# Kernel optimization log

Measured on AMD Instinct MI355X. Metric: run time of the kernel, lower is better.

The kernel has to match this reference:

```python
import jax, jax.numpy as jnp
import numpy as np

N_BUILDINGS = 4096
NUM_CLUSTERS = 128
EMBED_DIM = 128
TEMPORAL_DIM = 24


def setup_inputs() -> dict:
    key = jax.random.key(0)
    ks = jax.random.split(key, 12)
    E, N, C, T = EMBED_DIM, N_BUILDINGS, NUM_CLUSTERS, TEMPORAL_DIM

    def lin(k, fi, fo):
        k1, k2 = jax.random.split(k)
        w = jax.random.normal(k1, (fo, fi), jnp.float32) / np.sqrt(fi).astype(np.float32)
        b = jax.random.normal(k2, (fo,), jnp.float32) * 0.01
        return w, b

    fp_w1, fp_b1 = lin(ks[0], 2 * E + 2, 128)
    fp_w2, fp_b2 = lin(ks[1], 128, 64)
    fp_w3, fp_b3 = lin(ks[2], 64, 1)
    en_w1, en_b1 = lin(ks[3], 1, 16)
    en_w2, en_b2 = lin(ks[4], 16, 1)
    ps_w1, ps_b1 = lin(ks[5], E, 32)
    ps_w2, ps_b2 = lin(ks[6], 32, 1)

    embeddings = jax.random.normal(ks[7], (1, N, E), jnp.float32)
    generation = jax.random.uniform(ks[8], (1, N, T), jnp.float32) * 50.0
    consumption = jax.random.uniform(ks[9], (1, N, T), jnp.float32) * 50.0
    positions = jax.random.uniform(ks[10], (1, N, 2), jnp.float32) * 1000.0
    cluster_assignments = (jnp.arange(N) % C)[None, :].astype(jnp.int32)

    return dict(embeddings=embeddings, generation=generation, consumption=consumption,
                positions=positions,
                fp_w1=fp_w1, fp_b1=fp_b1, fp_w2=fp_w2, fp_b2=fp_b2, fp_w3=fp_w3, fp_b3=fp_b3,
                en_w1=en_w1, en_b1=en_b1, en_w2=en_w2, en_b2=en_b2,
                ps_w1=ps_w1, ps_b1=ps_b1, ps_w2=ps_w2, ps_b2=ps_b2,
                cluster_assignments=cluster_assignments, num_clusters=C, current_hour=12)


def _greedy_cluster(net0, prio, effm, pf):
    """Greedy allocation within one cluster. net0,prio: [K]; effm,pf: [K,K].
    Surplus rows and deficit cols are both visited in descending priority order;
    non-surplus rows have avail=0 and non-deficit cols have needed<=0, matching the
    original code's subset selection + break/continue semantics."""
    K = net0.shape[0]
    order = jnp.argsort(-prio)
    inv = jnp.argsort(order)
    net_o = net0[order]
    eff_o = effm[order][:, order]
    pf_o = pf[order][:, order]

    def outer(dnet, i):
        avail0 = jnp.maximum(net_o[i], 0.0)  # surplus net is never mutated

        def inner(carry, j):
            avail, dn = carry
            needed = -dn[j]
            active = (avail > 0.0) & (needed > 0.0)
            f = jnp.where(active, jnp.minimum(jnp.minimum(avail, needed), pf_o[i, j]), 0.0)
            dn = dn.at[j].add(f * eff_o[i, j])  # deficit receives delivered flow
            return (avail - f, dn), (f, active)

        (_, dnet), (frow, arow) = jax.lax.scan(inner, (avail0, dnet), jnp.arange(K))
        return dnet, (frow, arow)

    dnet, (flows_o, act_o) = jax.lax.scan(outer, net_o, jnp.arange(K))
    return flows_o[inv][:, inv], act_o[inv][:, inv], dnet[inv]


def _forward(embeddings, generation, consumption, positions,
             fp_w1, fp_b1, fp_w2, fp_b2, fp_w3, fp_b3,
             en_w1, en_b1, en_w2, en_b2,
             ps_w1, ps_b1, ps_w2, ps_b2,
             cluster_assignments, num_clusters, current_hour):
    B, N, E = embeddings.shape
    C = num_clusters
    K = N // C
    net = generation[0, :, current_hour] - consumption[0, :, current_hour]  # [N]

    g = jnp.argsort(cluster_assignments[0]).reshape(C, K)  # [C,K] building ids per cluster
    emb_c = embeddings[0][g]   # [C,K,E]
    pos_c = positions[0][g]    # [C,K,2]
    net_c = net[g]             # [C,K]

    # priority scorer (eval mode)
    h = jax.nn.relu(emb_c @ ps_w1.T + ps_b1)
    prio_c = jax.nn.sigmoid(h @ ps_w2.T + ps_b2)[..., 0]  # [C,K]

    # pairwise distances within cluster
    dist = jnp.linalg.norm(pos_c[:, :, None, :] - pos_c[:, None, :, :], axis=-1)  # [C,K,K]

    # efficiency net: eff = 0.85 + 0.13*sigmoid(MLP(dist/1000))
    eh = jax.nn.relu((dist / 1000.0)[..., None] * en_w1[:, 0] + en_b1)  # [C,K,K,16]
    eff = 0.85 + 0.13 * jax.nn.sigmoid(eh @ en_w2.T + en_b2)[..., 0]    # [C,K,K]

    # flow predictor on concat([emb_i, emb_j, dist, hour/24]); split W1 to avoid
    # materializing the [C,K,K,2E+2] feature tensor. Dropout is eval-mode identity.
    W1a, W1b = fp_w1[:, :E], fp_w1[:, E:2 * E]
    w1d, w1h = fp_w1[:, 2 * E], fp_w1[:, 2 * E + 1]
    hi = emb_c @ W1a.T  # [C,K,128]
    hj = emb_c @ W1b.T  # [C,K,128]
    hour_f = current_hour / 24.0
    h1 = jax.nn.relu(hi[:, :, None, :] + hj[:, None, :, :] + dist[..., None] * w1d + hour_f * w1h + fp_b1)
    h2 = jax.nn.relu(h1 @ fp_w2.T + fp_b2)
    pflow = jax.nn.softplus(h2 @ fp_w3.T + fp_b3)[..., 0]  # [C,K,K]

    flows_c, act_c, dnet_c = jax.vmap(_greedy_cluster)(net_c, prio_c, eff, pflow)

    sharing = jnp.zeros((N, N), embeddings.dtype).at[g[:, :, None], g[:, None, :]].set(flows_c)
    effmat = jnp.ones((N, N), embeddings.dtype).at[g[:, :, None], g[:, None, :]].set(
        jnp.where(act_c, eff, 1.0))
    net_after = jnp.zeros((N,), embeddings.dtype).at[g].set(dnet_c)

    sharing = sharing[None]
    effmat = effmat[None]
    total_shared = sharing.sum()
    energy_sent = sharing.sum(axis=2)
    energy_received = (sharing * effmat).sum(axis=1)
    return sharing, effmat, total_shared, energy_sent, energy_received, net_after[None]


def reference(embeddings, generation, consumption, positions,
              fp_w1, fp_b1, fp_w2, fp_b2, fp_w3, fp_b3,
              en_w1, en_b1, en_w2, en_b2,
              ps_w1, ps_b1, ps_w2, ps_b2,
              cluster_assignments, num_clusters, current_hour):
    return _forward(embeddings, generation, consumption, positions,
                    fp_w1, fp_b1, fp_w2, fp_b2, fp_w3, fp_b3,
                    en_w1, en_b1, en_w2, en_b2,
                    ps_w1, ps_b1, ps_w2, ps_b2,
                    cluster_assignments, num_clusters, current_hour)
```

## Files before the change

### kernel.cpp

```cpp
#include <hip/hip_runtime.h>
#include <math.h>

#define NB 4096
#define NC 128
#define NK 32
#define NE 128

typedef __bf16 bf16x8 __attribute__((ext_vector_type(8)));
typedef float floatx4 __attribute__((ext_vector_type(4)));

__device__ __forceinline__ float sigmoidf_(float x){
  if (x >= 0.f){ float z = expf(-x); return 1.f/(1.f+z); }
  float z = expf(x); return z/(1.f+z);
}
__device__ __forceinline__ float softplusf_(float x){
  return fmaxf(x, 0.f) + log1pf(expf(-fabsf(x)));
}
__device__ __forceinline__ unsigned int pack_bf16(float a, float b){
  unsigned short ua = __builtin_bit_cast(unsigned short, (__bf16)a);
  unsigned short ub = __builtin_bit_cast(unsigned short, (__bf16)b);
  return (unsigned int)ua | ((unsigned int)ub << 16);
}

__global__ void k_prep_group(const float* __restrict__ fp_w1, const float* __restrict__ ps_w1,
                             const float* __restrict__ fp_b1, const float* __restrict__ fp_w2,
                             const int* __restrict__ assign, const int* __restrict__ hourp,
                             float* __restrict__ w1at, float* __restrict__ w1bt,
                             float* __restrict__ ps_w1t, int* __restrict__ g,
                             int* __restrict__ row_of, float* __restrict__ w1d_c,
                             float* __restrict__ bzc, uint4* __restrict__ w2f,
                             float* __restrict__ total){
  int bid = blockIdx.x;
  int t = threadIdx.x;
  if (bid < 80){
    int idx = bid*256 + t;
    if (idx < 128*128){
      int o = idx >> 7, e = idx & 127;
      w1at[e*128 + o] = fp_w1[o*258 + e];
      w1bt[e*128 + o] = fp_w1[o*258 + 128 + e];
    } else {
      int i2 = idx - 128*128;
      if (i2 < 128*32){
        int e = i2 >> 5, q = i2 & 31;
        ps_w1t[e*32 + q] = ps_w1[q*128 + e];
      }
    }
  } else if (bid < 96){
    __shared__ int hist[NC];
    __shared__ int loc[256];
    int start = (bid - 80)*256;
    for (int c = t; c < NC; c += 256) hist[c] = 0;
    __syncthreads();
    for (int j = t; j < start; j += 256) atomicAdd(&hist[assign[j]], 1);
    int i = start + t;
    int c = assign[i];
    loc[t] = c;
    __syncthreads();
    int r = hist[c];
    for (int j = 0; j < 256; ++j) r += (j < t && loc[j] == c) ? 1 : 0;
    if (r >= NK) r = NK - 1;
    g[c*NK + r] = i;
    row_of[i] = c*NK + r;
  } else if (bid == 96){
    if (t < 128){
      float hour_f = (float)hourp[0] / 24.0f;
      w1d_c[t] = fp_w1[t*258 + 256];
      bzc[t]   = fmaf(hour_f, fp_w1[t*258 + 257], fp_b1[t]);
    }
    if (t == 128) total[0] = 0.f;
  } else {
    for (int ff = t; ff < 1024; ff += 256){
      int lane = ff & 63, fi = ff >> 6;
      int nt = fi >> 2, ks = fi & 3;
      int o = nt*16 + (lane & 15);
      int kb = ks*32 + (lane >> 4)*8;
      const float* src = fp_w2 + o*128 + kb;
      uint4 u;
      u.x = pack_bf16(src[0], src[1]);
      u.y = pack_bf16(src[2], src[3]);
      u.z = pack_bf16(src[4], src[5]);
      u.w = pack_bf16(src[6], src[7]);
      w2f[ff] = u;
    }
  }
}

__global__ void k_prio(const float* __restrict__ emb, const float* __restrict__ gen,
                       const float* __restrict__ cons, const float* __restrict__ pos,
                       const float* __restrict__ ps_w1t, const float* __restrict__ ps_b1,
                       const float* __restrict__ ps_w2, const float* __restrict__ ps_b2,
                       const int* __restrict__ row_of, const int* __restrict__ hourp,
                       float* __restrict__ net_c, float* __restrict__ prio_c,
                       float* __restrict__ pos_c){
  __shared__ float es[8*128];
  __shared__ float ws[128*32];
  int t = threadIdx.x;
  int i0 = blockIdx.x*8;
  for (int idx = t; idx < 8*128; idx += 256) es[idx] = emb[i0*128 + idx];
  for (int idx = t; idx < 128*32; idx += 256) ws[idx] = ps_w1t[idx];
  __syncthreads();
  int bl = t >> 5, q = t & 31;
  int i = i0 + bl;
  float acc = ps_b1[q];
  const float* er = &es[bl*128];
  for (int e = 0; e < 128; ++e) acc = fmaf(er[e], ws[e*32 + q], acc);
  float v = fmaxf(acc, 0.f) * ps_w2[q];
  for (int m = 16; m >= 1; m >>= 1) v += __shfl_xor(v, m, 32);
  if (q == 0){
    int ck = row_of[i];
    prio_c[ck] = sigmoidf_(v + ps_b2[0]);
    int h = hourp[0];
    net_c[ck] = gen[i*24 + h] - cons[i*24 + h];
    pos_c[2*ck]   = pos[2*i];
    pos_c[2*ck+1] = pos[2*i+1];
  }
}

__global__ void k_hij(const float* __restrict__ emb, const float* __restrict__ w1at,
                      const float* __restrict__ w1bt, const int* __restrict__ row_of,
                      float* __restrict__ hi_c, float* __restrict__ hj_c){
  __shared__ float es[16*132];
  int t = threadIdx.x;
  int i0 = blockIdx.x*16;
  for (int idx = t; idx < 16*128; idx += 256){
    int b = idx >> 7, e = idx & 127;
    es[b*132 + e] = emb[(i0 + b)*128 + e];
  }
  __syncthreads();
  int o = t & 127, half = t >> 7;
  float ai[8], aj[8];
#pragma unroll
  for (int r = 0; r < 8; ++r){ ai[r] = 0.f; aj[r] = 0.f; }
  for (int e = 0; e < 128; e += 4){
    float wa0 = w1at[(e+0)*128 + o], wa1 = w1at[(e+1)*128 + o];
    float wa2 = w1at[(e+2)*128 + o], wa3 = w1at[(e+3)*128 + o];
    float wb0 = w1bt[(e+0)*128 + o], wb1 = w1bt[(e+1)*128 + o];
    float wb2 = w1bt[(e+2)*128 + o], wb3 = w1bt[(e+3)*128 + o];
#pragma unroll
    for (int r = 0; r < 8; ++r){
      float4 ev = *(const float4*)&es[(half*8 + r)*132 + e];
      ai[r] = fmaf(ev.x, wa0, fmaf(ev.y, wa1, fmaf(ev.z, wa2, fmaf(ev.w, wa3, ai[r]))));
      aj[r] = fmaf(ev.x, wb0, fmaf(ev.y, wb1, fmaf(ev.z, wb2, fmaf(ev.w, wb3, aj[r]))));
    }
  }
#pragma unroll
  for (int r = 0; r < 8; ++r){
    int b = i0 + half*8 + r;
    int ck = row_of[b];
    hi_c[ck*128 + o] = ai[r];
    hj_c[ck*128 + o] = aj[r];
  }
}

__global__ __launch_bounds__(256) void k_pflow(
    const float* __restrict__ hi_c, const float* __restrict__ hj_c,
    const float* __restrict__ pos_c, const float* __restrict__ w1d_c,
    const float* __restrict__ bzc, const uint4* __restrict__ w2f,
    const float* __restrict__ fp_b2, const float* __restrict__ fp_w3,
    const float* __restrict__ fp_b3, float* __restrict__ pflow){
  int t = threadIdx.x;
  int lane = t & 63, wv = t >> 6;
  int gw = blockIdx.x*4 + wv;
  int c = gw >> 6;
  int rem = gw & 63;
  int i = rem >> 1, j0 = (rem & 1)*16;
  int l16 = lane & 15, quad = lane >> 4;
  int j = j0 + l16;
  float xi = pos_c[(c*NK + i)*2 + 0], yi = pos_c[(c*NK + i)*2 + 1];
  float xj = pos_c[(c*NK + j)*2 + 0], yj = pos_c[(c*NK + j)*2 + 1];
  float dx = xi - xj, dy = yi - yj;
  float d = sqrtf(fmaf(dx, dx, dy*dy));
  const float4* hi4 = (const float4*)(hi_c + (c*NK + i)*128);
  const float4* hj4 = (const float4*)(hj_c + (c*NK + j)*128);
  const float4* wd4 = (const float4*)w1d_c;
  const float4* bz4 = (const float4*)bzc;
  bf16x8 af[4];
#pragma unroll
  for (int ks = 0; ks < 4; ++ks){
    int q8 = ks*8 + quad*2;
    float4 a0 = hi4[q8], a1 = hi4[q8 + 1];
    float4 b0 = hj4[q8], b1 = hj4[q8 + 1];
    float4 w0 = wd4[q8], w1 = wd4[q8 + 1];
    float4 z0 = bz4[q8], z1 = bz4[q8 + 1];
    float v0 = fmaxf(a0.x + b0.x + fmaf(d, w0.x, z0.x), 0.f);
    float v1 = fmaxf(a0.y + b0.y + fmaf(d, w0.y, z0.y), 0.f);
    float v2 = fmaxf(a0.z + b0.z + fmaf(d, w0.z, z0.z), 0.f);
    float v3 = fmaxf(a0.w + b0.w + fmaf(d, w0.w, z0.w), 0.f);
    float v4 = fmaxf(a1.x + b1.x + fmaf(d, w1.x, z1.x), 0.f);
    float v5 = fmaxf(a1.y + b1.y + fmaf(d, w1.y, z1.y), 0.f);
    float v6 = fmaxf(a1.z + b1.z + fmaf(d, w1.z, z1.z), 0.f);
    float v7 = fmaxf(a1.w + b1.w + fmaf(d, w1.w, z1.w), 0.f);
    uint4 u;
    u.x = pack_bf16(v0, v1);
    u.y = pack_bf16(v2, v3);
    u.z = pack_bf16(v4, v5);
    u.w = pack_bf16(v6, v7);
    af[ks] = __builtin_bit_cast(bf16x8, u);
  }
  bf16x8 bfr[4][4];
#pragma unroll
  for (int nt = 0; nt < 4; ++nt)
#pragma unroll
    for (int ks = 0; ks < 4; ++ks)
      bfr[nt][ks] = __builtin_bit_cast(bf16x8, w2f[(nt*4 + ks)*64 + lane]);
  floatx4 acc[4];
#pragma unroll
  for (int nt = 0; nt < 4; ++nt){
    acc[nt] = (floatx4){0.f, 0.f, 0.f, 0.f};
#pragma unroll
    for (int ks = 0; ks < 4; ++ks)
      acc[nt] = __builtin_amdgcn_mfma_f32_16x16x32_bf16(af[ks], bfr[nt][ks], acc[nt], 0, 0, 0);
  }
  float b2v[4], w3v[4];
#pragma unroll
  for (int nt = 0; nt < 4; ++nt){
    b2v[nt] = fp_b2[nt*16 + l16];
    w3v[nt] = fp_w3[nt*16 + l16];
  }
  float b3 = fp_b3[0];
#pragma unroll
  for (int r = 0; r < 4; ++r){
    float s = 0.f;
#pragma unroll
    for (int nt = 0; nt < 4; ++nt)
      s = fmaf(fmaxf(acc[nt][r] + b2v[nt], 0.f), w3v[nt], s);
#pragma unroll
    for (int m = 8; m >= 1; m >>= 1) s += __shfl_xor(s, m);
    if (l16 == 0)
      pflow[c*1024 + i*32 + j0 + quad*4 + r] = softplusf_(s + b3);
  }
}

__global__ __launch_bounds__(64) void k_greedy(
    const float* __restrict__ net_c, const float* __restrict__ prio_c,
    const float* __restrict__ pos_c, const float* __restrict__ en_w1,
    const float* __restrict__ en_b1, const float* __restrict__ en_w2,
    const float* __restrict__ en_b2, const float* __restrict__ pflow,
    const int* __restrict__ g,
    float* __restrict__ fl_c, float* __restrict__ ef_c, float* __restrict__ total,
    float* __restrict__ esent, float* __restrict__ erecv, float* __restrict__ nafter){
  __shared__ float pf_s[1024];
  __shared__ float ef_s[1024];
  __shared__ float fl_s[1024];
  __shared__ float efm_s[1024];
  __shared__ float px[32], py[32];
  __shared__ int order_s[32];
  __shared__ int gl[32];
  int t = threadIdx.x;
  int tl = t & 31;
  int c = blockIdx.x;
  for (int e = t; e < 1024; e += 64) pf_s[e] = pflow[c*1024 + e];
  if (t < 32){
    float2 p2 = ((const float2*)pos_c)[c*NK + t];
    px[t] = p2.x; py[t] = p2.y;
    gl[t] = g[c*NK + t];
  }
  __syncthreads();
  for (int e = t; e < 1024; e += 64){
    int ii = e >> 5, jj = e & 31;
    float dx = px[ii] - px[jj], dy = py[ii] - py[jj];
    float d = sqrtf(fmaf(dx, dx, dy*dy));
    float ds = d * (1.0f/1000.0f);
    float acc = en_b2[0];
#pragma unroll
    for (int q = 0; q < 16; ++q)
      acc = fmaf(fmaxf(fmaf(ds, en_w1[q], en_b1[q]), 0.f), en_w2[q], acc);
    ef_s[e] = 0.85f + 0.13f*sigmoidf_(acc);
  }
  float p = (t < 32) ? prio_c[c*NK + t] : -1e30f;
  int rank = 0;
  for (int k = 0; k < 32; ++k){
    float pk = __shfl(p, k, 32);
    rank += ((pk > p) || (pk == p && k < tl)) ? 1 : 0;
  }
  if (t < 32) order_s[rank] = t;
  __syncthreads();
  int b = order_s[tl];
  float net0 = net_c[c*NK + b];
  float dnet = net0;
  float recv = 0.f;
  float ctotal = 0.f;
  for (int i = 0; i < 32; ++i){
    int a = order_s[i];
    float av0 = fmaxf(__shfl(net0, i, 32), 0.f);
    float pf = pf_s[a*32 + b];
    float ef = ef_s[a*32 + b];
    float needed = -dnet;
    float m = (needed > 0.f) ? fminf(needed, pf) : 0.f;
    float s = m;
#pragma unroll
    for (int dd = 1; dd < 32; dd <<= 1){
      float u = __shfl_up(s, dd, 32);
      if (tl >= dd) s += u;
    }
    float Se = __shfl_up(s, 1, 32);
    if (tl == 0) Se = 0.f;
    float rprev = fmaxf(av0 - Se, 0.f);
    int act = (rprev > 0.f) && (needed > 0.f);
    float f = fminf(m, rprev);
    dnet = fmaf(f, ef, dnet);
    recv = fmaf(f, ef, recv);
    if (t < 32){
      fl_s[a*32 + b]  = f;
      efm_s[a*32 + b] = act ? ef : 1.0f;
    }
    float rs = f;
    for (int mm = 16; mm >= 1; mm >>= 1) rs += __shfl_xor(rs, mm, 32);
    if (t == 0){ esent[gl[a]] = rs; ctotal += rs; }
  }
  if (t < 32){
    nafter[gl[b]] = dnet;
    erecv[gl[b]]  = recv;
  }
  if (t == 0) atomicAdd(total, ctotal);
  __syncthreads();
  for (int e = t; e < 1024; e += 64){
    fl_c[c*1024 + e] = fl_s[e];
    ef_c[c*1024 + e] = efm_s[e];
  }
}

__global__ __launch_bounds__(256) void k_write(
    const float* __restrict__ fl_c, const float* __restrict__ ef_c,
    const int* __restrict__ g, const int* __restrict__ row_of,
    float* __restrict__ sharing, float* __restrict__ effm){
  __shared__ float rowS[4096];
  __shared__ float rowE[4096];
  __shared__ int   cols[32];
  __shared__ float vals[32];
  __shared__ float vale[32];
  int t = threadIdx.x;
  int r = blockIdx.x;
  int ra = row_of[r];
  int c = ra >> 5, a = ra & 31;
  if (t < 32){
    cols[t] = g[c*NK + t];
    vals[t] = fl_c[c*1024 + a*32 + t];
    vale[t] = ef_c[c*1024 + a*32 + t];
  }
  float4 z4 = make_float4(0.f, 0.f, 0.f, 0.f);
  float4 o4 = make_float4(1.f, 1.f, 1.f, 1.f);
  float4* s4 = (float4*)rowS;
  float4* e4 = (float4*)rowE;
#pragma unroll
  for (int q = 0; q < 4; ++q){ s4[t + 256*q] = z4; e4[t + 256*q] = o4; }
  __syncthreads();
  if (t < 32){ rowS[cols[t]] = vals[t]; rowE[cols[t]] = vale[t]; }
  __syncthreads();
  float4* gs = (float4*)(sharing + (long)r*NB);
  float4* ge = (float4*)(effm    + (long)r*NB);
#pragma unroll
  for (int q = 0; q < 4; ++q){ gs[t + 256*q] = s4[t + 256*q]; ge[t + 256*q] = e4[t + 256*q]; }
}

extern "C" void kernel_launch(void* const* d_in, const int* in_sizes, int n_in,
                              void* d_out, int out_size, void* d_ws, size_t ws_size,
                              hipStream_t stream){
  (void)in_sizes; (void)n_in; (void)out_size; (void)ws_size;
  const float* emb   = (const float*)d_in[0];
  const float* gen   = (const float*)d_in[1];
  const float* cons  = (const float*)d_in[2];
  const float* pos   = (const float*)d_in[3];
  const float* fp_w1 = (const float*)d_in[4];
  const float* fp_b1 = (const float*)d_in[5];
  const float* fp_w2 = (const float*)d_in[6];
  const float* fp_b2 = (const float*)d_in[7];
  const float* fp_w3 = (const float*)d_in[8];
  const float* fp_b3 = (const float*)d_in[9];
  const float* en_w1 = (const float*)d_in[10];
  const float* en_b1 = (const float*)d_in[11];
  const float* en_w2 = (const float*)d_in[12];
  const float* en_b2 = (const float*)d_in[13];
  const float* ps_w1 = (const float*)d_in[14];
  const float* ps_b1 = (const float*)d_in[15];
  const float* ps_w2 = (const float*)d_in[16];
  const float* ps_b2 = (const float*)d_in[17];
  const int*   assign = (const int*)d_in[18];
  const int*   hourp  = (const int*)d_in[20];

  char* ws = (char*)d_ws;
  float* w1at   = (float*)(ws + 0);
  float* w1bt   = (float*)(ws + 65536);
  float* ps_w1t = (float*)(ws + 131072);
  int*   g      = (int*)  (ws + 147456);
  int*   row_of = (int*)  (ws + 163840);
  float* net_c  = (float*)(ws + 180224);
  float* prio_c = (float*)(ws + 196608);
  float* pos_c  = (float*)(ws + 212992);
  float* w1d_c  = (float*)(ws + 245760);
  float* bzc    = (float*)(ws + 246272);
  float* hi_c   = (float*)(ws + 262144);
  float* hj_c   = (float*)(ws + 2359296);
  float* pflow  = (float*)(ws + 4456448);
  float* fl_c   = (float*)(ws + 4980736);
  float* ef_c   = (float*)(ws + 5505024);
  uint4* w2f    = (uint4*)(ws + 6029312);

  float* sharing = (float*)d_out;
  float* effm    = sharing + (long)NB*NB;
  float* total   = effm + (long)NB*NB;
  float* esent   = total + 1;
  float* erecv   = esent + NB;
  float* nafter  = erecv + NB;

  hipLaunchKernelGGL(k_prep_group, dim3(98), dim3(256), 0, stream,
                     fp_w1, ps_w1, fp_b1, fp_w2, assign, hourp,
                     w1at, w1bt, ps_w1t, g, row_of, w1d_c, bzc, w2f, total);
  hipLaunchKernelGGL(k_prio, dim3(512), dim3(256), 0, stream,
                     emb, gen, cons, pos, ps_w1t, ps_b1, ps_w2, ps_b2,
                     row_of, hourp, net_c, prio_c, pos_c);
  hipLaunchKernelGGL(k_hij, dim3(256), dim3(256), 0, stream,
                     emb, w1at, w1bt, row_of, hi_c, hj_c);
  hipLaunchKernelGGL(k_pflow, dim3(2048), dim3(256), 0, stream,
                     hi_c, hj_c, pos_c, w1d_c, bzc, w2f, fp_b2, fp_w3, fp_b3,
                     pflow);
  hipLaunchKernelGGL(k_greedy, dim3(128), dim3(64), 0, stream,
                     net_c, prio_c, pos_c, en_w1, en_b1, en_w2, en_b2, pflow, g,
                     fl_c, ef_c, total, esent, erecv, nafter);
  hipLaunchKernelGGL(k_write, dim3(4096), dim3(256), 0, stream,
                     fl_c, ef_c, g, row_of, sharing, effm);
}
```

Baseline: 267.5 us.

## Fuse priority, hidden projection, pair-flow MLP and greedy into one per-cluster kernel

Merges k_prio, k_hij, k_pflow and k_greedy into a single k_cluster kernel with one 256-thread block per cluster. Each block gathers its 32 buildings, computes priority, the hi/hj projections into shared memory, the pairwise MFMA flow MLP into shared memory, and then runs the greedy allocation. This removes three launches and the global round trips for hi_c, hj_c, pflow, net_c and prio_c. In exchange only 128 blocks run, so the projection and MLP stages have much less parallelism and may leave most CUs idle.

```diff
diff --git a/kernel.cpp b/kernel.cpp
--- a/kernel.cpp
+++ b/kernel.cpp
@@ -85,178 +85,172 @@
   }
 }
 
-__global__ void k_prio(const float* __restrict__ emb, const float* __restrict__ gen,
-                       const float* __restrict__ cons, const float* __restrict__ pos,
-                       const float* __restrict__ ps_w1t, const float* __restrict__ ps_b1,
-                       const float* __restrict__ ps_w2, const float* __restrict__ ps_b2,
-                       const int* __restrict__ row_of, const int* __restrict__ hourp,
-                       float* __restrict__ net_c, float* __restrict__ prio_c,
-                       float* __restrict__ pos_c){
-  __shared__ float es[8*128];
-  __shared__ float ws[128*32];
-  int t = threadIdx.x;
-  int i0 = blockIdx.x*8;
-  for (int idx = t; idx < 8*128; idx += 256) es[idx] = emb[i0*128 + idx];
-  for (int idx = t; idx < 128*32; idx += 256) ws[idx] = ps_w1t[idx];
-  __syncthreads();
-  int bl = t >> 5, q = t & 31;
-  int i = i0 + bl;
-  float acc = ps_b1[q];
-  const float* er = &es[bl*128];
-  for (int e = 0; e < 128; ++e) acc = fmaf(er[e], ws[e*32 + q], acc);
-  float v = fmaxf(acc, 0.f) * ps_w2[q];
-  for (int m = 16; m >= 1; m >>= 1) v += __shfl_xor(v, m, 32);
-  if (q == 0){
-    int ck = row_of[i];
-    prio_c[ck] = sigmoidf_(v + ps_b2[0]);
-    int h = hourp[0];
-    net_c[ck] = gen[i*24 + h] - cons[i*24 + h];
-    pos_c[2*ck]   = pos[2*i];
-    pos_c[2*ck+1] = pos[2*i+1];
-  }
-}
-
-__global__ void k_hij(const float* __restrict__ emb, const float* __restrict__ w1at,
-                      const float* __restrict__ w1bt, const int* __restrict__ row_of,
-                      float* __restrict__ hi_c, float* __restrict__ hj_c){
-  __shared__ float es[16*132];
-  int t = threadIdx.x;
-  int i0 = blockIdx.x*16;
-  for (int idx = t; idx < 16*128; idx += 256){
-    int b = idx >> 7, e = idx & 127;
-    es[b*132 + e] = emb[(i0 + b)*128 + e];
-  }
-  __syncthreads();
-  int o = t & 127, half = t >> 7;
-  float ai[8], aj[8];
-#pragma unroll
-  for (int r = 0; r < 8; ++r){ ai[r] = 0.f; aj[r] = 0.f; }
-  for (int e = 0; e < 128; e += 4){
-    float wa0 = w1at[(e+0)*128 + o], wa1 = w1at[(e+1)*128 + o];
-    float wa2 = w1at[(e+2)*128 + o], wa3 = w1at[(e+3)*128 + o];
-    float wb0 = w1bt[(e+0)*128 + o], wb1 = w1bt[(e+1)*128 + o];
-    float wb2 = w1bt[(e+2)*128 + o], wb3 = w1bt[(e+3)*128 + o];
-#pragma unroll
-    for (int r = 0; r < 8; ++r){
-      float4 ev = *(const float4*)&es[(half*8 + r)*132 + e];
-      ai[r] = fmaf(ev.x, wa0, fmaf(ev.y, wa1, fmaf(ev.z, wa2, fmaf(ev.w, wa3, ai[r]))));
-      aj[r] = fmaf(ev.x, wb0, fmaf(ev.y, wb1, fmaf(ev.z, wb2, fmaf(ev.w, wb3, aj[r]))));
-    }
-  }
-#pragma unroll
-  for (int r = 0; r < 8; ++r){
-    int b = i0 + half*8 + r;
-    int ck = row_of[b];
-    hi_c[ck*128 + o] = ai[r];
-    hj_c[ck*128 + o] = aj[r];
-  }
-}
-
-__global__ __launch_bounds__(256) void k_pflow(
-    const float* __restrict__ hi_c, const float* __restrict__ hj_c,
-    const float* __restrict__ pos_c, const float* __restrict__ w1d_c,
-    const float* __restrict__ bzc, const uint4* __restrict__ w2f,
-    const float* __restrict__ fp_b2, const float* __restrict__ fp_w3,
-    const float* __restrict__ fp_b3, float* __restrict__ pflow){
-  int t = threadIdx.x;
-  int lane = t & 63, wv = t >> 6;
-  int gw = blockIdx.x*4 + wv;
-  int c = gw >> 6;
-  int rem = gw & 63;
-  int i = rem >> 1, j0 = (rem & 1)*16;
-  int l16 = lane & 15, quad = lane >> 4;
-  int j = j0 + l16;
-  float xi = pos_c[(c*NK + i)*2 + 0], yi = pos_c[(c*NK + i)*2 + 1];
-  float xj = pos_c[(c*NK + j)*2 + 0], yj = pos_c[(c*NK + j)*2 + 1];
-  float dx = xi - xj, dy = yi - yj;
-  float d = sqrtf(fmaf(dx, dx, dy*dy));
-  const float4* hi4 = (const float4*)(hi_c + (c*NK + i)*128);
-  const float4* hj4 = (const float4*)(hj_c + (c*NK + j)*128);
-  const float4* wd4 = (const float4*)w1d_c;
-  const float4* bz4 = (const float4*)bzc;
-  bf16x8 af[4];
-#pragma unroll
-  for (int ks = 0; ks < 4; ++ks){
-    int q8 = ks*8 + quad*2;
-    float4 a0 = hi4[q8], a1 = hi4[q8 + 1];
-    float4 b0 = hj4[q8], b1 = hj4[q8 + 1];
-    float4 w0 = wd4[q8], w1 = wd4[q8 + 1];
-    float4 z0 = bz4[q8], z1 = bz4[q8 + 1];
-    float v0 = fmaxf(a0.x + b0.x + fmaf(d, w0.x, z0.x), 0.f);
-    float v1 = fmaxf(a0.y + b0.y + fmaf(d, w0.y, z0.y), 0.f);
-    float v2 = fmaxf(a0.z + b0.z + fmaf(d, w0.z, z0.z), 0.f);
-    float v3 = fmaxf(a0.w + b0.w + fmaf(d, w0.w, z0.w), 0.f);
-    float v4 = fmaxf(a1.x + b1.x + fmaf(d, w1.x, z1.x), 0.f);
-    float v5 = fmaxf(a1.y + b1.y + fmaf(d, w1.y, z1.y), 0.f);
-    float v6 = fmaxf(a1.z + b1.z + fmaf(d, w1.z, z1.z), 0.f);
-    float v7 = fmaxf(a1.w + b1.w + fmaf(d, w1.w, z1.w), 0.f);
-    uint4 u;
-    u.x = pack_bf16(v0, v1);
-    u.y = pack_bf16(v2, v3);
-    u.z = pack_bf16(v4, v5);
-    u.w = pack_bf16(v6, v7);
-    af[ks] = __builtin_bit_cast(bf16x8, u);
-  }
-  bf16x8 bfr[4][4];
-#pragma unroll
-  for (int nt = 0; nt < 4; ++nt)
-#pragma unroll
-    for (int ks = 0; ks < 4; ++ks)
-      bfr[nt][ks] = __builtin_bit_cast(bf16x8, w2f[(nt*4 + ks)*64 + lane]);
-  floatx4 acc[4];
-#pragma unroll
-  for (int nt = 0; nt < 4; ++nt){
-    acc[nt] = (floatx4){0.f, 0.f, 0.f, 0.f};
-#pragma unroll
-    for (int ks = 0; ks < 4; ++ks)
-      acc[nt] = __builtin_amdgcn_mfma_f32_16x16x32_bf16(af[ks], bfr[nt][ks], acc[nt], 0, 0, 0);
-  }
-  float b2v[4], w3v[4];
-#pragma unroll
-  for (int nt = 0; nt < 4; ++nt){
-    b2v[nt] = fp_b2[nt*16 + l16];
-    w3v[nt] = fp_w3[nt*16 + l16];
-  }
-  float b3 = fp_b3[0];
-#pragma unroll
-  for (int r = 0; r < 4; ++r){
-    float s = 0.f;
-#pragma unroll
-    for (int nt = 0; nt < 4; ++nt)
-      s = fmaf(fmaxf(acc[nt][r] + b2v[nt], 0.f), w3v[nt], s);
-#pragma unroll
-    for (int m = 8; m >= 1; m >>= 1) s += __shfl_xor(s, m);
-    if (l16 == 0)
-      pflow[c*1024 + i*32 + j0 + quad*4 + r] = softplusf_(s + b3);
-  }
-}
-
-__global__ __launch_bounds__(64) void k_greedy(
-    const float* __restrict__ net_c, const float* __restrict__ prio_c,
-    const float* __restrict__ pos_c, const float* __restrict__ en_w1,
-    const float* __restrict__ en_b1, const float* __restrict__ en_w2,
-    const float* __restrict__ en_b2, const float* __restrict__ pflow,
-    const int* __restrict__ g,
+__global__ __launch_bounds__(256, 1) void k_cluster(
+    const float* __restrict__ emb, const float* __restrict__ gen,
+    const float* __restrict__ cons, const float* __restrict__ pos,
+    const float* __restrict__ ps_w1t, const float* __restrict__ ps_b1,
+    const float* __restrict__ ps_w2, const float* __restrict__ ps_b2,
+    const float* __restrict__ w1at, const float* __restrict__ w1bt,
+    const float* __restrict__ w1d_c, const float* __restrict__ bzc,
+    const uint4* __restrict__ w2f, const float* __restrict__ fp_b2,
+    const float* __restrict__ fp_w3, const float* __restrict__ fp_b3,
+    const float* __restrict__ en_w1, const float* __restrict__ en_b1,
+    const float* __restrict__ en_w2, const float* __restrict__ en_b2,
+    const int* __restrict__ g, const int* __restrict__ hourp,
     float* __restrict__ fl_c, float* __restrict__ ef_c, float* __restrict__ total,
     float* __restrict__ esent, float* __restrict__ erecv, float* __restrict__ nafter){
+  __shared__ float his[32*128];
+  __shared__ float hjs[32*132];
   __shared__ float pf_s[1024];
   __shared__ float ef_s[1024];
-  __shared__ float fl_s[1024];
-  __shared__ float efm_s[1024];
-  __shared__ float px[32], py[32];
+  __shared__ float px[32], py[32], netl[32], prio_l[32];
+  __shared__ int gl[32];
   __shared__ int order_s[32];
-  __shared__ int gl[32];
   int t = threadIdx.x;
-  int tl = t & 31;
   int c = blockIdx.x;
-  for (int e = t; e < 1024; e += 64) pf_s[e] = pflow[c*1024 + e];
+  int lane = t & 63, wv = t >> 6;
+
   if (t < 32){
-    float2 p2 = ((const float2*)pos_c)[c*NK + t];
-    px[t] = p2.x; py[t] = p2.y;
-    gl[t] = g[c*NK + t];
-  }
-  __syncthreads();
-  for (int e = t; e < 1024; e += 64){
+    int b = g[c*NK + t];
+    gl[t] = b;
+    px[t] = pos[2*b];
+    py[t] = pos[2*b + 1];
+    int h = hourp[0];
+    netl[t] = gen[b*24 + h] - cons[b*24 + h];
+  }
+  __syncthreads();
+
+  {
+    int q = t & 31;
+    int bsub = t >> 5;
+    for (int bb = 0; bb < 4; ++bb){
+      int b = bb*8 + bsub;
+      const float* er = emb + gl[b]*128;
+      float acc = ps_b1[q];
+      for (int e = 0; e < 128; ++e) acc = fmaf(er[e], ps_w1t[e*32 + q], acc);
+      float v = fmaxf(acc, 0.f) * ps_w2[q];
+      for (int m = 16; m >= 1; m >>= 1) v += __shfl_xor(v, m, 32);
+      if (q == 0) prio_l[b] = sigmoidf_(v + ps_b2[0]);
+    }
+  }
+
+  {
+    int r0 = wv*8;
+    int gr[8];
+#pragma unroll
+    for (int r = 0; r < 8; ++r) gr[r] = gl[r0 + r];
+    float a0[8], a1[8], c0[8], c1[8];
+#pragma unroll
+    for (int r = 0; r < 8; ++r){ a0[r]=0.f; a1[r]=0.f; c0[r]=0.f; c1[r]=0.f; }
+    for (int e = 0; e < 128; e += 4){
+      float wa00 = w1at[(e+0)*128 + lane],      wa01 = w1at[(e+1)*128 + lane];
+      float wa02 = w1at[(e+2)*128 + lane],      wa03 = w1at[(e+3)*128 + lane];
+      float wa10 = w1at[(e+0)*128 + lane + 64], wa11 = w1at[(e+1)*128 + lane + 64];
+      float wa12 = w1at[(e+2)*128 + lane + 64], wa13 = w1at[(e+3)*128 + lane + 64];
+      float wb00 = w1bt[(e+0)*128 + lane],      wb01 = w1bt[(e+1)*128 + lane];
+      float wb02 = w1bt[(e+2)*128 + lane],      wb03 = w1bt[(e+3)*128 + lane];
+      float wb10 = w1bt[(e+0)*128 + lane + 64], wb11 = w1bt[(e+1)*128 + lane + 64];
+      float wb12 = w1bt[(e+2)*128 + lane + 64], wb13 = w1bt[(e+3)*128 + lane + 64];
+#pragma unroll
+      for (int r = 0; r < 8; ++r){
+        float4 ev = *(const float4*)&emb[gr[r]*128 + e];
+        a0[r] = fmaf(ev.x, wa00, fmaf(ev.y, wa01, fmaf(ev.z, wa02, fmaf(ev.w, wa03, a0[r]))));
+        a1[r] = fmaf(ev.x, wa10, fmaf(ev.y, wa11, fmaf(ev.z, wa12, fmaf(ev.w, wa13, a1[r]))));
+        c0[r] = fmaf(ev.x, wb00, fmaf(ev.y, wb01, fmaf(ev.z, wb02, fmaf(ev.w, wb03, c0[r]))));
+        c1[r] = fmaf(ev.x, wb10, fmaf(ev.y, wb11, fmaf(ev.z, wb12, fmaf(ev.w, wb13, c1[r]))));
+      }
+    }
+#pragma unroll
+    for (int r = 0; r < 8; ++r){
+      his[(r0+r)*128 + lane]      = a0[r];
+      his[(r0+r)*128 + lane + 64] = a1[r];
+      hjs[(r0+r)*132 + lane]      = c0[r];
+      hjs[(r0+r)*132 + lane + 64] = c1[r];
+    }
+  }
+  __syncthreads();
+
+  {
+    int l16 = lane & 15, quad = lane >> 4;
+    int j0 = (wv >> 1)*16;
+    int j = j0 + l16;
+    bf16x8 bfr[4][4];
+#pragma unroll
+    for (int nt = 0; nt < 4; ++nt)
+#pragma unroll
+      for (int ks = 0; ks < 4; ++ks)
+        bfr[nt][ks] = __builtin_bit_cast(bf16x8, w2f[(nt*4 + ks)*64 + lane]);
+    float4 hjv[8], wdv[8], bzv[8];
+#pragma unroll
+    for (int ks = 0; ks < 4; ++ks){
+      int q8 = ks*8 + quad*2;
+      hjv[ks*2+0] = *(const float4*)&hjs[j*132 + q8*4];
+      hjv[ks*2+1] = *(const float4*)&hjs[j*132 + q8*4 + 4];
+      wdv[ks*2+0] = ((const float4*)w1d_c)[q8];
+      wdv[ks*2+1] = ((const float4*)w1d_c)[q8 + 1];
+      bzv[ks*2+0] = ((const float4*)bzc)[q8];
+      bzv[ks*2+1] = ((const float4*)bzc)[q8 + 1];
+    }
+    float b2v[4], w3v[4];
+#pragma unroll
+    for (int nt = 0; nt < 4; ++nt){
+      b2v[nt] = fp_b2[nt*16 + l16];
+      w3v[nt] = fp_w3[nt*16 + l16];
+    }
+    float b3 = fp_b3[0];
+    float xj = px[j], yj = py[j];
+    for (int it = 0; it < 16; ++it){
+      int i = (wv & 1) + it*2;
+      float dx = px[i] - xj, dy = py[i] - yj;
+      float d = sqrtf(fmaf(dx, dx, dy*dy));
+      bf16x8 af[4];
+#pragma unroll
+      for (int ks = 0; ks < 4; ++ks){
+        int q8 = ks*8 + quad*2;
+        float4 h0 = *(const float4*)&his[i*128 + q8*4];
+        float4 h1 = *(const float4*)&his[i*128 + q8*4 + 4];
+        float4 j0v = hjv[ks*2], j1v = hjv[ks*2+1];
+        float4 w0 = wdv[ks*2], w1 = wdv[ks*2+1];
+        float4 z0 = bzv[ks*2], z1 = bzv[ks*2+1];
+        float v0 = fmaxf(h0.x + j0v.x + fmaf(d, w0.x, z0.x), 0.f);
+        float v1 = fmaxf(h0.y + j0v.y + fmaf(d, w0.y, z0.y), 0.f);
+        float v2 = fmaxf(h0.z + j0v.z + fmaf(d, w0.z, z0.z), 0.f);
+        float v3 = fmaxf(h0.w + j0v.w + fmaf(d, w0.w, z0.w), 0.f);
+        float v4 = fmaxf(h1.x + j1v.x + fmaf(d, w1.x, z1.x), 0.f);
+        float v5 = fmaxf(h1.y + j1v.y + fmaf(d, w1.y, z1.y), 0.f);
+        float v6 = fmaxf(h1.z + j1v.z + fmaf(d, w1.z, z1.z), 0.f);
+        float v7 = fmaxf(h1.w + j1v.w + fmaf(d, w1.w, z1.w), 0.f);
+        uint4 u;
+        u.x = pack_bf16(v0, v1);
+        u.y = pack_bf16(v2, v3);
+        u.z = pack_bf16(v4, v5);
+        u.w = pack_bf16(v6, v7);
+        af[ks] = __builtin_bit_cast(bf16x8, u);
+      }
+      floatx4 acc[4];
+#pragma unroll
+      for (int nt = 0; nt < 4; ++nt){
+        acc[nt] = (floatx4){0.f, 0.f, 0.f, 0.f};
+#pragma unroll
+        for (int ks = 0; ks < 4; ++ks)
+          acc[nt] = __builtin_amdgcn_mfma_f32_16x16x32_bf16(af[ks], bfr[nt][ks], acc[nt], 0, 0, 0);
+      }
+#pragma unroll
+      for (int r = 0; r < 4; ++r){
+        float s = 0.f;
+#pragma unroll
+        for (int nt = 0; nt < 4; ++nt)
+          s = fmaf(fmaxf(acc[nt][r] + b2v[nt], 0.f), w3v[nt], s);
+#pragma unroll
+        for (int m = 8; m >= 1; m >>= 1) s += __shfl_xor(s, m);
+        if (l16 == 0)
+          pf_s[i*32 + j0 + quad*4 + r] = softplusf_(s + b3);
+      }
+    }
+  }
+  __syncthreads();
+
+  for (int e = t; e < 1024; e += 256){
     int ii = e >> 5, jj = e & 31;
     float dx = px[ii] - px[jj], dy = py[ii] - py[jj];
     float d = sqrtf(fmaf(dx, dx, dy*dy));
@@ -267,56 +261,58 @@
       acc = fmaf(fmaxf(fmaf(ds, en_w1[q], en_b1[q]), 0.f), en_w2[q], acc);
     ef_s[e] = 0.85f + 0.13f*sigmoidf_(acc);
   }
-  float p = (t < 32) ? prio_c[c*NK + t] : -1e30f;
-  int rank = 0;
-  for (int k = 0; k < 32; ++k){
-    float pk = __shfl(p, k, 32);
-    rank += ((pk > p) || (pk == p && k < tl)) ? 1 : 0;
-  }
-  if (t < 32) order_s[rank] = t;
-  __syncthreads();
-  int b = order_s[tl];
-  float net0 = net_c[c*NK + b];
-  float dnet = net0;
-  float recv = 0.f;
-  float ctotal = 0.f;
-  for (int i = 0; i < 32; ++i){
-    int a = order_s[i];
-    float av0 = fmaxf(__shfl(net0, i, 32), 0.f);
-    float pf = pf_s[a*32 + b];
-    float ef = ef_s[a*32 + b];
-    float needed = -dnet;
-    float m = (needed > 0.f) ? fminf(needed, pf) : 0.f;
-    float s = m;
-#pragma unroll
-    for (int dd = 1; dd < 32; dd <<= 1){
-      float u = __shfl_up(s, dd, 32);
-      if (tl >= dd) s += u;
-    }
-    float Se = __shfl_up(s, 1, 32);
-    if (tl == 0) Se = 0.f;
-    float rprev = fmaxf(av0 - Se, 0.f);
-    int act = (rprev > 0.f) && (needed > 0.f);
-    float f = fminf(m, rprev);
-    dnet = fmaf(f, ef, dnet);
-    recv = fmaf(f, ef, recv);
+  if (t < 64){
+    int tl = t & 31;
+    float p = (t < 32) ? prio_l[t] : -1e30f;
+    int rank = 0;
+    for (int k = 0; k < 32; ++k){
+      float pk = __shfl(p, k, 32);
+      rank += ((pk > p) || (pk == p && k < tl)) ? 1 : 0;
+    }
+    if (t < 32) order_s[rank] = t;
+  }
+  __syncthreads();
+
+  if (t < 64){
+    int tl = t & 31;
+    int b = order_s[tl];
+    float net0 = netl[b];
+    float dnet = net0;
+    float recv = 0.f;
+    float ctotal = 0.f;
+    for (int i = 0; i < 32; ++i){
+      int a = order_s[i];
+      float av0 = fmaxf(__shfl(net0, i, 32), 0.f);
+      float pf = pf_s[a*32 + b];
+      float ef = ef_s[a*32 + b];
+      float needed = -dnet;
+      float m = (needed > 0.f) ? fminf(needed, pf) : 0.f;
+      float s = m;
+#pragma unroll
+      for (int dd = 1; dd < 32; dd <<= 1){
+        float u = __shfl_up(s, dd, 32);
+        if (tl >= dd) s += u;
+      }
+      float Se = __shfl_up(s, 1, 32);
+      if (tl == 0) Se = 0.f;
+      float rprev = fmaxf(av0 - Se, 0.f);
+      int act = (rprev > 0.f) && (needed > 0.f);
+      float f = fminf(m, rprev);
+      dnet = fmaf(f, ef, dnet);
+      recv = fmaf(f, ef, recv);
+      if (t < 32){
+        fl_c[c*1024 + a*32 + b] = f;
+        ef_c[c*1024 + a*32 + b] = act ? ef : 1.0f;
+      }
+      float rs = f;
+      for (int mm = 16; mm >= 1; mm >>= 1) rs += __shfl_xor(rs, mm, 32);
+      if (t == 0){ esent[gl[a]] = rs; ctotal += rs; }
+    }
     if (t < 32){
-      fl_s[a*32 + b]  = f;
-      efm_s[a*32 + b] = act ? ef : 1.0f;
-    }
-    float rs = f;
-    for (int mm = 16; mm >= 1; mm >>= 1) rs += __shfl_xor(rs, mm, 32);
-    if (t == 0){ esent[gl[a]] = rs; ctotal += rs; }
-  }
-  if (t < 32){
-    nafter[gl[b]] = dnet;
-    erecv[gl[b]]  = recv;
-  }
-  if (t == 0) atomicAdd(total, ctotal);
-  __syncthreads();
-  for (int e = t; e < 1024; e += 64){
-    fl_c[c*1024 + e] = fl_s[e];
-    ef_c[c*1024 + e] = efm_s[e];
+      nafter[gl[b]] = dnet;
+      erecv[gl[b]]  = recv;
+    }
+    if (t == 0) atomicAdd(total, ctotal);
   }
 }
 
@@ -384,17 +380,11 @@
   float* ps_w1t = (float*)(ws + 131072);
   int*   g      = (int*)  (ws + 147456);
   int*   row_of = (int*)  (ws + 163840);
-  float* net_c  = (float*)(ws + 180224);
-  float* prio_c = (float*)(ws + 196608);
-  float* pos_c  = (float*)(ws + 212992);
-  float* w1d_c  = (float*)(ws + 245760);
-  float* bzc    = (float*)(ws + 246272);
-  float* hi_c   = (float*)(ws + 262144);
-  float* hj_c   = (float*)(ws + 2359296);
-  float* pflow  = (float*)(ws + 4456448);
-  float* fl_c   = (float*)(ws + 4980736);
-  float* ef_c   = (float*)(ws + 5505024);
-  uint4* w2f    = (uint4*)(ws + 6029312);
+  float* w1d_c  = (float*)(ws + 180224);
+  float* bzc    = (float*)(ws + 180736);
+  uint4* w2f    = (uint4*)(ws + 181248);
+  float* fl_c   = (float*)(ws + 262144);
+  float* ef_c   = (float*)(ws + 786432);
 
   float* sharing = (float*)d_out;
   float* effm    = sharing + (long)NB*NB;
@@ -406,16 +396,10 @@
   hipLaunchKernelGGL(k_prep_group, dim3(98), dim3(256), 0, stream,
                      fp_w1, ps_w1, fp_b1, fp_w2, assign, hourp,
                      w1at, w1bt, ps_w1t, g, row_of, w1d_c, bzc, w2f, total);
-  hipLaunchKernelGGL(k_prio, dim3(512), dim3(256), 0, stream,
+  hipLaunchKernelGGL(k_cluster, dim3(128), dim3(256), 0, stream,
                      emb, gen, cons, pos, ps_w1t, ps_b1, ps_w2, ps_b2,
-                     row_of, hourp, net_c, prio_c, pos_c);
-  hipLaunchKernelGGL(k_hij, dim3(256), dim3(256), 0, stream,
-                     emb, w1at, w1bt, row_of, hi_c, hj_c);
-  hipLaunchKernelGGL(k_pflow, dim3(2048), dim3(256), 0, stream,
-                     hi_c, hj_c, pos_c, w1d_c, bzc, w2f, fp_b2, fp_w3, fp_b3,
-                     pflow);
-  hipLaunchKernelGGL(k_greedy, dim3(128), dim3(64), 0, stream,
-                     net_c, prio_c, pos_c, en_w1, en_b1, en_w2, en_b2, pflow, g,
+                     w1at, w1bt, w1d_c, bzc, w2f, fp_b2, fp_w3, fp_b3,
+                     en_w1, en_b1, en_w2, en_b2, g, hourp,
                      fl_c, ef_c, total, esent, erecv, nafter);
   hipLaunchKernelGGL(k_write, dim3(4096), dim3(256), 0, stream,
                      fl_c, ef_c, g, row_of, sharing, effm);
```

Result: slower. 276.0 us (+3.2%).
